# Performance work log

Hardware: AMD Instinct MI355X
Metric: run time of the kernel (lower is better)

The kernel has to match this reference:

```python
import jax, jax.numpy as jnp
import numpy as np

N_QUBITS = 8
DEPTH = 2
N_STATES = 1 << N_QUBITS  # 256
BATCH = (2, 32768)


def _cz_phase(n_qubits: int) -> np.ndarray:
    """Diagonal phase of nearest-neighbor CZ gates over all basis states."""
    basis = np.arange(1 << n_qubits)
    phase = np.ones(1 << n_qubits, dtype=np.float32)
    for left in range(n_qubits - 1):
        both_one = ((basis >> left) & 1 == 1) & ((basis >> (left + 1)) & 1 == 1)
        phase = np.where(both_one, -phase, phase)
    return phase


def setup_inputs() -> dict:
    key = jax.random.key(0)
    k1, k2 = jax.random.split(key)
    projected_features = jax.random.normal(k1, BATCH + (N_QUBITS,), dtype=jnp.float32)
    theta = 0.05 * jax.random.normal(k2, (DEPTH, N_QUBITS), dtype=jnp.float32)
    input_scale = jnp.ones((N_QUBITS,), dtype=jnp.float32)
    return {"projected_features": projected_features, "theta": theta, "input_scale": input_scale}


def reference(projected_features, theta, input_scale):
    n_qubits = projected_features.shape[-1]
    depth = theta.shape[0]
    n_states = 1 << n_qubits
    batch_shape = projected_features.shape[:-1]
    dtype = projected_features.dtype

    cz_phase = jnp.asarray(_cz_phase(n_qubits), dtype=dtype)

    # |0...0> initial state
    state = jnp.zeros(batch_shape + (n_states,), dtype=dtype).at[..., 0].set(1.0)
    bounded = jnp.tanh(projected_features) * np.pi  # [..., n_qubits]

    for layer in range(depth):
        for q in range(n_qubits):
            angle = bounded[..., q] * input_scale[q] + theta[layer, q]  # [...]
            c = jnp.cos(angle * 0.5)[..., None, None]
            s = jnp.sin(angle * 0.5)[..., None, None]
            # basis index = high * 2^(q+1) + bit_q * 2^q + low; split out bit_q
            r = state.reshape(batch_shape + (n_states >> (q + 1), 2, 1 << q))
            s0 = r[..., 0, :]
            s1 = r[..., 1, :]
            new = jnp.stack([c * s0 - s * s1, s * s0 + c * s1], axis=-2)
            state = new.reshape(batch_shape + (n_states,))
        state = state * cz_phase

    norm = jnp.linalg.norm(state, axis=-1, keepdims=True)
    return state / jnp.maximum(norm, 1e-12)
```

## Files before the change

kernel.cpp:

```cpp
#include <hip/hip_runtime.h>
#include <math.h>

#define PI_F 3.14159265358979323846f

typedef float f32x4 __attribute__((ext_vector_type(4)));

template <int PAT>
__device__ __forceinline__ float swzf(float x) {
    return __int_as_float(__builtin_amdgcn_ds_swizzle(__float_as_int(x), PAT));
}
#define BCAST_PAT(q) (((((q) & 3) | (((q) & 4) << 1)) << 5) | 0x14)

template <int CTRL>
__device__ __forceinline__ float dppf(float x) {
    int i = __float_as_int(x);
    return __int_as_float(__builtin_amdgcn_update_dpp(i, i, CTRL, 0xF, 0xF, false));
}
#define DPP_XOR1 0xB1
#define DPP_XOR2 0x4E
#define DPP_XOR8 0x128

#define SLO_MASK 0x4748B848u

__global__ __launch_bounds__(256) void qenc_kernel(
    const float* __restrict__ pf,
    const float* __restrict__ theta,
    const float* __restrict__ scale,
    float* __restrict__ out,
    int B)
{
    const int lane = threadIdx.x & 63;
    const int wid  = threadIdx.x >> 6;
    const int sub  = (lane & 3) | ((lane >> 1) & 4);
    const int g    = ((lane >> 2) & 1) | ((lane >> 3) & 6);

    __shared__ __align__(16) float lds[4 * 2048];
    float* base = lds + wid * 2048;

    const int grp   = blockIdx.x * 4 + wid;
    const int bwave = grp * 8;
    const int b     = bwave + g;
    if (b >= B) return;

    float x  = pf[(size_t)b * 8 + sub];
    float e  = __expf(2.f * x);
    float th = 1.f - 2.f / (e + 1.f);
    float b2 = th * (0.5f * PI_F) * scale[sub];
    float h0 = b2 + 0.5f * theta[sub];
    float h1 = b2 + 0.5f * theta[8 + sub];
    float c0 = __cosf(h0), s0 = __sinf(h0);
    float cL = __cosf(h1), sL = __sinf(h1);

    float KC0 = swzf<BCAST_PAT(0)>(c0), KS0 = swzf<BCAST_PAT(0)>(s0);
    float KC1 = swzf<BCAST_PAT(1)>(c0), KS1 = swzf<BCAST_PAT(1)>(s0);
    float KC2 = swzf<BCAST_PAT(2)>(c0), KS2 = swzf<BCAST_PAT(2)>(s0);
    float KC3 = swzf<BCAST_PAT(3)>(c0), KS3 = swzf<BCAST_PAT(3)>(s0);
    float KC4 = swzf<BCAST_PAT(4)>(c0), KS4 = swzf<BCAST_PAT(4)>(s0);
    float KC5 = swzf<BCAST_PAT(5)>(c0), KS5 = swzf<BCAST_PAT(5)>(s0);
    float KC6 = swzf<BCAST_PAT(6)>(c0), KS6 = swzf<BCAST_PAT(6)>(s0);
    float KC7 = swzf<BCAST_PAT(7)>(c0), KS7 = swzf<BCAST_PAT(7)>(s0);

    const float A  = (__popc(sub & (sub >> 1) & 3) & 1) ? -1.f : 1.f;
    const float A4 = (sub & 1) ? -A : A;

    float f5 = (sub & 1) ? KS5 : KC5;
    float f6 = (sub & 2) ? KS6 : KC6;
    float f7 = (sub & 4) ? KS7 : KC7;
    float Phi = f5 * f6 * f7 * A;
    float KS4L = (sub & 1) ? -KS4 : KS4;

    float a00 = KC0 * KC1, a10 = KS0 * KC1, a01 = KC0 * KS1, a11 = KS0 * KS1;
    const float uu[4] = { Phi * a00, Phi * a10, Phi * a01, Phi * a11 };
    float t23_0 = KC2 * KC3, t23_1 = KS2 * KC3, t23_2 = KC2 * KS3, t23_3 = KS2 * KS3;
    const float wwl[8] = { t23_0 * KC4,  t23_1 * KC4,  t23_2 * KC4,  t23_3 * KC4,
                           t23_0 * KS4L, t23_1 * KS4L, t23_2 * KS4L, t23_3 * KS4L };

    float v[32];
#pragma unroll
    for (int i = 0; i < 32; ++i) {
        v[i] = ((SLO_MASK >> i) & 1) ? (-uu[i & 3] * wwl[i >> 2])
                                     : ( uu[i & 3] * wwl[i >> 2]);
    }

#define INTRA_GATE(SB, CG, SG)                                        \
    do {                                                              \
        _Pragma("unroll")                                             \
        for (int bse = 0; bse < 32; bse += 2 * (SB)) {                \
            _Pragma("unroll")                                         \
            for (int off = 0; off < (SB); ++off) {                    \
                int i0 = bse + off, i1 = i0 + (SB);                   \
                float a = v[i0], bb = v[i1];                          \
                v[i0] = fmaf((CG), a, -((SG) * bb));                  \
                v[i1] = fmaf((CG), bb, (SG) * a);                     \
            }                                                         \
        }                                                             \
    } while (0)

#define CROSS_GATE_DPP(CTRL, BIT, CG, SG)                             \
    do {                                                              \
        float se = (sub & (BIT)) ? (SG) : -(SG);                      \
        _Pragma("unroll")                                             \
        for (int i = 0; i < 32; ++i) {                                \
            float t = dppf<CTRL>(v[i]);                               \
            v[i] = fmaf((CG), v[i], se * t);                          \
        }                                                             \
    } while (0)

    {
        float cg, sg;
        cg = swzf<BCAST_PAT(1)>(cL); sg = swzf<BCAST_PAT(1)>(sL); INTRA_GATE(2,  cg, sg);
        cg = swzf<BCAST_PAT(2)>(cL); sg = swzf<BCAST_PAT(2)>(sL); INTRA_GATE(4,  cg, sg);
        cg = swzf<BCAST_PAT(3)>(cL); sg = swzf<BCAST_PAT(3)>(sL); INTRA_GATE(8,  cg, sg);
        cg = swzf<BCAST_PAT(4)>(cL); sg = swzf<BCAST_PAT(4)>(sL); INTRA_GATE(16, cg, sg);
        cg = swzf<BCAST_PAT(5)>(cL); sg = swzf<BCAST_PAT(5)>(sL); CROSS_GATE_DPP(DPP_XOR1, 1, cg, sg);
        cg = swzf<BCAST_PAT(6)>(cL); sg = swzf<BCAST_PAT(6)>(sL); CROSS_GATE_DPP(DPP_XOR2, 2, cg, sg);
        cg = swzf<BCAST_PAT(7)>(cL); sg = swzf<BCAST_PAT(7)>(sL); CROSS_GATE_DPP(DPP_XOR8, 4, cg, sg);

        cg = swzf<BCAST_PAT(0)>(cL); sg = swzf<BCAST_PAT(0)>(sL);
        float cA = cg * A,  sA = sg * A;
        float cB = cg * A4, sB = sg * A4;
#pragma unroll
        for (int j = 0; j < 16; ++j) {
            int i0 = 2 * j, i1 = i0 + 1;
            float C = (i0 & 16) ? cB : cA;
            float S = (i0 & 16) ? sB : sA;
            float a = v[i0], bb = v[i1];
            float t  = S * bb;
            float t2 = S * a;
            v[i0] = ((SLO_MASK >> i0) & 1) ? fmaf(-C, a, t)    : fmaf(C, a, -t);
            v[i1] = ((SLO_MASK >> i1) & 1) ? fmaf(-C, bb, -t2) : fmaf(C, bb, t2);
        }
    }


#pragma unroll
    for (int k = 0; k < 8; ++k) {
        int c  = sub * 8 + k;
        int cp = c ^ sub;
        f32x4 w = { v[4 * k], v[4 * k + 1], v[4 * k + 2], v[4 * k + 3] };
        *reinterpret_cast<f32x4*>(base + g * 256 + cp * 4) = w;
    }
    const int cr = lane ^ (lane >> 3);
#pragma unroll
    for (int j = 0; j < 8; ++j) {
        f32x4 t = *reinterpret_cast<const f32x4*>(base + j * 256 + cr * 4);
        __builtin_nontemporal_store(t,
            reinterpret_cast<f32x4*>(out + (size_t)(bwave + j) * 256 + lane * 4));
    }
}

extern "C" void kernel_launch(void* const* d_in, const int* in_sizes, int n_in,
                              void* d_out, int out_size, void* d_ws, size_t ws_size,
                              hipStream_t stream) {
    const float* pf    = (const float*)d_in[0];
    const float* theta = (const float*)d_in[1];
    const float* scale = (const float*)d_in[2];
    float* out = (float*)d_out;

    int B = in_sizes[0] / 8;
    int grid = (B / 8 + 3) / 4;
    qenc_kernel<<<grid, 256, 0, stream>>>(pf, theta, scale, out, B);
}
```

Before: 18.99 us.

## Switch state-vector gate math to packed fp16 pairs

Holds the 256-amplitude state as 16 packed half2 registers instead of 32 floats and applies the rotation gates with packed fp16 FMAs, so each swizzle and DPP moves two values at once. Cos/sin pairs are packed into one register before broadcasting, which halves the swizzle count. The qubit-0 gate becomes a packed swap-and-FMA, and the sign and phase fix-up moves to a final multiply. This cuts ALU and cross-lane work but loses accuracy: fp16 with round-toward-zero conversion may exceed the output tolerance, and the kernel is likely bound by output stores anyway.

```diff
diff --git a/kernel.cpp b/kernel.cpp
--- a/kernel.cpp
+++ b/kernel.cpp
@@ -3,22 +3,39 @@
 
 #define PI_F 3.14159265358979323846f
 
-typedef float f32x4 __attribute__((ext_vector_type(4)));
+typedef float    f32x4 __attribute__((ext_vector_type(4)));
+typedef _Float16 h2    __attribute__((ext_vector_type(2)));
+
+#if __has_builtin(__builtin_elementwise_fma)
+#define FMA2(a, b, c) __builtin_elementwise_fma((a), (b), (c))
+#else
+#define FMA2(a, b, c) ((a) * (b) + (c))
+#endif
+
+__device__ __forceinline__ h2 pkrtz(float a, float b) {
+    return __builtin_bit_cast(h2, __builtin_amdgcn_cvt_pkrtz(a, b));
+}
 
 template <int PAT>
-__device__ __forceinline__ float swzf(float x) {
-    return __int_as_float(__builtin_amdgcn_ds_swizzle(__float_as_int(x), PAT));
+__device__ __forceinline__ h2 swzh(h2 x) {
+    return __builtin_bit_cast(h2, __builtin_amdgcn_ds_swizzle(__builtin_bit_cast(int, x), PAT));
 }
 #define BCAST_PAT(q) (((((q) & 3) | (((q) & 4) << 1)) << 5) | 0x14)
 
 template <int CTRL>
-__device__ __forceinline__ float dppf(float x) {
-    int i = __float_as_int(x);
-    return __int_as_float(__builtin_amdgcn_update_dpp(i, i, CTRL, 0xF, 0xF, false));
+__device__ __forceinline__ h2 dpph(h2 x) {
+    int i = __builtin_bit_cast(int, x);
+    return __builtin_bit_cast(h2, __builtin_amdgcn_update_dpp(i, i, CTRL, 0xF, 0xF, false));
 }
 #define DPP_XOR1 0xB1
 #define DPP_XOR2 0x4E
 #define DPP_XOR8 0x128
+
+__device__ __forceinline__ h2 hswap(h2 a) {
+    return __builtin_shufflevector(a, a, 1, 0);
+}
+__device__ __forceinline__ h2 splat_lo(h2 a) { h2 r = { a[0], a[0] }; return r; }
+__device__ __forceinline__ h2 splat_hi(h2 a) { h2 r = { a[1], a[1] }; return r; }
 
 #define SLO_MASK 0x4748B848u
 
@@ -46,19 +63,25 @@
     float e  = __expf(2.f * x);
     float th = 1.f - 2.f / (e + 1.f);
     float b2 = th * (0.5f * PI_F) * scale[sub];
-    float h0 = b2 + 0.5f * theta[sub];
-    float h1 = b2 + 0.5f * theta[8 + sub];
-    float c0 = __cosf(h0), s0 = __sinf(h0);
-    float cL = __cosf(h1), sL = __sinf(h1);
+    float h0a = b2 + 0.5f * theta[sub];
+    float h1a = b2 + 0.5f * theta[8 + sub];
+    float c0 = __cosf(h0a), s0 = __sinf(h0a);
+    float cL = __cosf(h1a), sL = __sinf(h1a);
+    h2 cs0 = pkrtz(c0, s0);
+    h2 csl = pkrtz(cL, sL);
 
-    float KC0 = swzf<BCAST_PAT(0)>(c0), KS0 = swzf<BCAST_PAT(0)>(s0);
-    float KC1 = swzf<BCAST_PAT(1)>(c0), KS1 = swzf<BCAST_PAT(1)>(s0);
-    float KC2 = swzf<BCAST_PAT(2)>(c0), KS2 = swzf<BCAST_PAT(2)>(s0);
-    float KC3 = swzf<BCAST_PAT(3)>(c0), KS3 = swzf<BCAST_PAT(3)>(s0);
-    float KC4 = swzf<BCAST_PAT(4)>(c0), KS4 = swzf<BCAST_PAT(4)>(s0);
-    float KC5 = swzf<BCAST_PAT(5)>(c0), KS5 = swzf<BCAST_PAT(5)>(s0);
-    float KC6 = swzf<BCAST_PAT(6)>(c0), KS6 = swzf<BCAST_PAT(6)>(s0);
-    float KC7 = swzf<BCAST_PAT(7)>(c0), KS7 = swzf<BCAST_PAT(7)>(s0);
+    h2 k0 = swzh<BCAST_PAT(0)>(cs0), k1 = swzh<BCAST_PAT(1)>(cs0);
+    h2 k2 = swzh<BCAST_PAT(2)>(cs0), k3 = swzh<BCAST_PAT(3)>(cs0);
+    h2 k4 = swzh<BCAST_PAT(4)>(cs0), k5 = swzh<BCAST_PAT(5)>(cs0);
+    h2 k6 = swzh<BCAST_PAT(6)>(cs0), k7 = swzh<BCAST_PAT(7)>(cs0);
+    float KC0 = (float)k0[0], KS0 = (float)k0[1];
+    float KC1 = (float)k1[0], KS1 = (float)k1[1];
+    float KC2 = (float)k2[0], KS2 = (float)k2[1];
+    float KC3 = (float)k3[0], KS3 = (float)k3[1];
+    float KC4 = (float)k4[0], KS4 = (float)k4[1];
+    float KC5 = (float)k5[0], KS5 = (float)k5[1];
+    float KC6 = (float)k6[0], KS6 = (float)k6[1];
+    float KC7 = (float)k7[0], KS7 = (float)k7[1];
 
     const float A  = (__popc(sub & (sub >> 1) & 3) & 1) ? -1.f : 1.f;
     const float A4 = (sub & 1) ? -A : A;
@@ -66,7 +89,7 @@
     float f5 = (sub & 1) ? KS5 : KC5;
     float f6 = (sub & 2) ? KS6 : KC6;
     float f7 = (sub & 4) ? KS7 : KC7;
-    float Phi = f5 * f6 * f7 * A;
+    float Phi  = f5 * f6 * f7 * A;
     float KS4L = (sub & 1) ? -KS4 : KS4;
 
     float a00 = KC0 * KC1, a10 = KS0 * KC1, a01 = KC0 * KS1, a11 = KS0 * KS1;
@@ -75,69 +98,77 @@
     const float wwl[8] = { t23_0 * KC4,  t23_1 * KC4,  t23_2 * KC4,  t23_3 * KC4,
                            t23_0 * KS4L, t23_1 * KS4L, t23_2 * KS4L, t23_3 * KS4L };
 
-    float v[32];
+    h2 P[16];
 #pragma unroll
-    for (int i = 0; i < 32; ++i) {
-        v[i] = ((SLO_MASK >> i) & 1) ? (-uu[i & 3] * wwl[i >> 2])
-                                     : ( uu[i & 3] * wwl[i >> 2]);
+    for (int j = 0; j < 16; ++j) {
+        float lo = uu[2 * (j & 1)]     * wwl[j >> 1];
+        float hi = uu[2 * (j & 1) + 1] * wwl[j >> 1];
+        if ((SLO_MASK >> (2 * j)) & 1)     lo = -lo;
+        if ((SLO_MASK >> (2 * j + 1)) & 1) hi = -hi;
+        P[j] = pkrtz(lo, hi);
     }
 
-#define INTRA_GATE(SB, CG, SG)                                        \
+    h2 q0 = swzh<BCAST_PAT(0)>(csl), q1 = swzh<BCAST_PAT(1)>(csl);
+    h2 q2 = swzh<BCAST_PAT(2)>(csl), q3 = swzh<BCAST_PAT(3)>(csl);
+    h2 q4 = swzh<BCAST_PAT(4)>(csl), q5 = swzh<BCAST_PAT(5)>(csl);
+    h2 q6 = swzh<BCAST_PAT(6)>(csl), q7 = swzh<BCAST_PAT(7)>(csl);
+
+#define PK_INTRA(SBJ, cs)                                             \
     do {                                                              \
+        h2 c2 = splat_lo(cs), s2 = splat_hi(cs);                      \
         _Pragma("unroll")                                             \
-        for (int bse = 0; bse < 32; bse += 2 * (SB)) {                \
+        for (int bse = 0; bse < 16; bse += 2 * (SBJ)) {               \
             _Pragma("unroll")                                         \
-            for (int off = 0; off < (SB); ++off) {                    \
-                int i0 = bse + off, i1 = i0 + (SB);                   \
-                float a = v[i0], bb = v[i1];                          \
-                v[i0] = fmaf((CG), a, -((SG) * bb));                  \
-                v[i1] = fmaf((CG), bb, (SG) * a);                     \
+            for (int off = 0; off < (SBJ); ++off) {                   \
+                int j0 = bse + off, j1 = j0 + (SBJ);                  \
+                h2 a = P[j0], bb = P[j1];                             \
+                P[j0] = FMA2(c2, a, -(s2 * bb));                      \
+                P[j1] = FMA2(c2, bb, s2 * a);                         \
             }                                                         \
         }                                                             \
     } while (0)
 
-#define CROSS_GATE_DPP(CTRL, BIT, CG, SG)                             \
+#define PK_CROSS(CTRL, BIT, cs)                                       \
     do {                                                              \
-        float se = (sub & (BIT)) ? (SG) : -(SG);                      \
+        h2 c2 = splat_lo(cs), s2 = splat_hi(cs);                      \
+        h2 se = (sub & (BIT)) ? s2 : -s2;                             \
         _Pragma("unroll")                                             \
-        for (int i = 0; i < 32; ++i) {                                \
-            float t = dppf<CTRL>(v[i]);                               \
-            v[i] = fmaf((CG), v[i], se * t);                          \
+        for (int j = 0; j < 16; ++j) {                                \
+            h2 t = dpph<CTRL>(P[j]);                                  \
+            P[j] = FMA2(c2, P[j], se * t);                            \
         }                                                             \
     } while (0)
 
+    PK_INTRA(1, q1);
+    PK_INTRA(2, q2);
+    PK_INTRA(4, q3);
+    PK_INTRA(8, q4);
+    PK_CROSS(DPP_XOR1, 1, q5);
+    PK_CROSS(DPP_XOR2, 2, q6);
+    PK_CROSS(DPP_XOR8, 4, q7);
     {
-        float cg, sg;
-        cg = swzf<BCAST_PAT(1)>(cL); sg = swzf<BCAST_PAT(1)>(sL); INTRA_GATE(2,  cg, sg);
-        cg = swzf<BCAST_PAT(2)>(cL); sg = swzf<BCAST_PAT(2)>(sL); INTRA_GATE(4,  cg, sg);
-        cg = swzf<BCAST_PAT(3)>(cL); sg = swzf<BCAST_PAT(3)>(sL); INTRA_GATE(8,  cg, sg);
-        cg = swzf<BCAST_PAT(4)>(cL); sg = swzf<BCAST_PAT(4)>(sL); INTRA_GATE(16, cg, sg);
-        cg = swzf<BCAST_PAT(5)>(cL); sg = swzf<BCAST_PAT(5)>(sL); CROSS_GATE_DPP(DPP_XOR1, 1, cg, sg);
-        cg = swzf<BCAST_PAT(6)>(cL); sg = swzf<BCAST_PAT(6)>(sL); CROSS_GATE_DPP(DPP_XOR2, 2, cg, sg);
-        cg = swzf<BCAST_PAT(7)>(cL); sg = swzf<BCAST_PAT(7)>(sL); CROSS_GATE_DPP(DPP_XOR8, 4, cg, sg);
-
-        cg = swzf<BCAST_PAT(0)>(cL); sg = swzf<BCAST_PAT(0)>(sL);
-        float cA = cg * A,  sA = sg * A;
-        float cB = cg * A4, sB = sg * A4;
+        h2 c2 = splat_lo(q0);
+        _Float16 sh = q0[1];
+        h2 sm = { (_Float16)(-sh), sh };
 #pragma unroll
-        for (int j = 0; j < 16; ++j) {
-            int i0 = 2 * j, i1 = i0 + 1;
-            float C = (i0 & 16) ? cB : cA;
-            float S = (i0 & 16) ? sB : sA;
-            float a = v[i0], bb = v[i1];
-            float t  = S * bb;
-            float t2 = S * a;
-            v[i0] = ((SLO_MASK >> i0) & 1) ? fmaf(-C, a, t)    : fmaf(C, a, -t);
-            v[i1] = ((SLO_MASK >> i1) & 1) ? fmaf(-C, bb, -t2) : fmaf(C, bb, t2);
-        }
+        for (int j = 0; j < 16; ++j)
+            P[j] = FMA2(c2, P[j], sm * hswap(P[j]));
     }
 
+#pragma unroll
+    for (int j = 0; j < 16; ++j) {
+        float bA = (j < 8) ? A : A4;
+        h2 sv = { (_Float16)(((SLO_MASK >> (2 * j)) & 1) ? -bA : bA),
+                  (_Float16)(((SLO_MASK >> (2 * j + 1)) & 1) ? -bA : bA) };
+        P[j] = P[j] * sv;
+    }
 
 #pragma unroll
     for (int k = 0; k < 8; ++k) {
         int c  = sub * 8 + k;
         int cp = c ^ sub;
-        f32x4 w = { v[4 * k], v[4 * k + 1], v[4 * k + 2], v[4 * k + 3] };
+        f32x4 w = { (float)P[2 * k][0], (float)P[2 * k][1],
+                    (float)P[2 * k + 1][0], (float)P[2 * k + 1][1] };
         *reinterpret_cast<f32x4*>(base + g * 256 + cp * 4) = w;
     }
     const int cr = lane ^ (lane >> 3);
```

Result: faster. 18.15 us (-4.4%).
